# Optimization experiments

Measured on AMD Instinct MI355X. Metric: run time of the kernel, lower is better.

Reference implementation:

```python
import jax, jax.numpy as jnp
import numpy as np

EMBED_DIM = 256
NUM_HEADS = 8
HEAD_DIM = EMBED_DIM // NUM_HEADS
FFN_DIM = 4 * EMBED_DIM
B, N = 2, 2048


def _layernorm(x, w, b, eps=1e-5):
    mu = jnp.mean(x, axis=-1, keepdims=True)
    var = jnp.var(x, axis=-1, keepdims=True)
    return (x - mu) * jax.lax.rsqrt(var + eps) * w + b


def setup_inputs() -> dict:
    key = jax.random.key(0)
    ks = jax.random.split(key, 16)
    s = 0.02
    d = {
        "x": jax.random.normal(ks[0], (B, N, EMBED_DIM), jnp.float32),
        "influence_matrix": jax.random.uniform(ks[1], (B, N, N), jnp.float32),
        "qw": jax.random.normal(ks[2], (EMBED_DIM, EMBED_DIM), jnp.float32) * s,
        "qb": jnp.zeros((EMBED_DIM,), jnp.float32),
        "kw": jax.random.normal(ks[3], (EMBED_DIM, EMBED_DIM), jnp.float32) * s,
        "kb": jnp.zeros((EMBED_DIM,), jnp.float32),
        "vw": jax.random.normal(ks[4], (EMBED_DIM, EMBED_DIM), jnp.float32) * s,
        "vb": jnp.zeros((EMBED_DIM,), jnp.float32),
        "ow": jax.random.normal(ks[5], (EMBED_DIM, EMBED_DIM), jnp.float32) * s,
        "ob": jnp.zeros((EMBED_DIM,), jnp.float32),
        "w1": jax.random.normal(ks[6], (EMBED_DIM, FFN_DIM), jnp.float32) * s,
        "b1": jnp.zeros((FFN_DIM,), jnp.float32),
        "w2": jax.random.normal(ks[7], (FFN_DIM, EMBED_DIM), jnp.float32) * s,
        "b2": jnp.zeros((EMBED_DIM,), jnp.float32),
        "ln1_w": jnp.ones((EMBED_DIM,), jnp.float32),
        "ln1_b": jnp.zeros((EMBED_DIM,), jnp.float32),
        "ln2_w": jnp.ones((EMBED_DIM,), jnp.float32),
        "ln2_b": jnp.zeros((EMBED_DIM,), jnp.float32),
    }
    return d


def reference(x, influence_matrix, qw, qb, kw, kb, vw, vb, ow, ob,
              w1, b1, w2, b2, ln1_w, ln1_b, ln2_w, ln2_b):
    # --- pre-norm attention with multiplicative influence bias ---
    h = _layernorm(x, ln1_w, ln1_b)
    q = (h @ qw + qb).reshape(B, N, NUM_HEADS, HEAD_DIM)
    k = (h @ kw + kb).reshape(B, N, NUM_HEADS, HEAD_DIM)
    v = (h @ vw + vb).reshape(B, N, NUM_HEADS, HEAD_DIM)
    scores = jnp.einsum('bnhd,bmhd->bhnm', q, k) / np.sqrt(HEAD_DIM).astype(np.float32)
    scores = scores * (1.0 + influence_matrix[:, None, :, :])  # multiplicative bias
    attn = jax.nn.softmax(scores, axis=-1)
    out = jnp.einsum('bhnm,bmhd->bnhd', attn, v).reshape(B, N, EMBED_DIM)
    x = x + out @ ow + ob
    # --- GELU FFN (torch GELU is exact erf form) ---
    h2 = _layernorm(x, ln2_w, ln2_b)
    ff = jax.nn.gelu(h2 @ w1 + b1, approximate=False) @ w2 + b2
    return x + ff
```

## Files before the change

kernel.cpp:

```cpp
#include <hip/hip_runtime.h>
#include <hip/hip_bf16.h>
#include <math.h>

#define NSEQ 2048
#define DMODEL 256

typedef __attribute__((ext_vector_type(8))) __bf16 bf16x8;
typedef __attribute__((ext_vector_type(4))) float f32x4;
typedef __attribute__((ext_vector_type(8))) unsigned short ushort8;
typedef __attribute__((ext_vector_type(4))) unsigned int uint4e;

__device__ __forceinline__ unsigned short f2b(float f) {
    return __builtin_bit_cast(unsigned short, (__bf16)f);
}
__device__ __forceinline__ float b2f(unsigned short u) {
    return (float)__builtin_bit_cast(__bf16, u);
}
__device__ __forceinline__ bf16x8 ldfrag16(const void* p) {
    return __builtin_bit_cast(bf16x8, *(const uint4e*)p);
}

__global__ __launch_bounds__(256)
void tr_kernel(const float* __restrict__ in, __bf16* __restrict__ out, int K, int N)
{
    __shared__ float tile[32][33];
    const int tx = threadIdx.x & 31, ty = threadIdx.x >> 5;
    const int n0 = blockIdx.x * 32, k0 = blockIdx.y * 32;
#pragma unroll
    for (int j = 0; j < 4; ++j)
        tile[ty * 4 + j][tx] = in[(size_t)(k0 + ty * 4 + j) * N + n0 + tx];
    __syncthreads();
#pragma unroll
    for (int j = 0; j < 4; ++j)
        out[(size_t)(n0 + ty * 4 + j) * K + k0 + tx] = (__bf16)tile[tx][ty * 4 + j];
}

__global__ __launch_bounds__(256)
void tr4_kernel(const float* __restrict__ w0, const float* __restrict__ w1,
                const float* __restrict__ w2, const float* __restrict__ w3,
                __bf16* __restrict__ o0, __bf16* __restrict__ o1,
                __bf16* __restrict__ o2, __bf16* __restrict__ o3)
{
    __shared__ float tile[32][33];
    const int z = blockIdx.z;
    const float* in = (z == 0) ? w0 : (z == 1) ? w1 : (z == 2) ? w2 : w3;
    __bf16* out     = (z == 0) ? o0 : (z == 1) ? o1 : (z == 2) ? o2 : o3;
    const int tx = threadIdx.x & 31, ty = threadIdx.x >> 5;
    const int n0 = blockIdx.x * 32, k0 = blockIdx.y * 32;
#pragma unroll
    for (int j = 0; j < 4; ++j)
        tile[ty * 4 + j][tx] = in[(size_t)(k0 + ty * 4 + j) * 256 + n0 + tx];
    __syncthreads();
#pragma unroll
    for (int j = 0; j < 4; ++j)
        out[(size_t)(n0 + ty * 4 + j) * 256 + k0 + tx] = (__bf16)tile[tx][ty * 4 + j];
}

__global__ __launch_bounds__(256)
void ln_kernel(const float* __restrict__ x, const float* __restrict__ g,
               const float* __restrict__ b, __bf16* __restrict__ out)
{
    const int row  = blockIdx.x * 4 + (threadIdx.x >> 6);
    const int lane = threadIdx.x & 63;
    const float4 v = *(const float4*)(x + (size_t)row * DMODEL + lane * 4);
    float s  = v.x + v.y + v.z + v.w;
    float s2 = v.x*v.x + v.y*v.y + v.z*v.z + v.w*v.w;
#pragma unroll
    for (int off = 32; off; off >>= 1) {
        s  += __shfl_xor(s, off);
        s2 += __shfl_xor(s2, off);
    }
    const float mu = s * (1.0f / DMODEL);
    const float rs = rsqrtf(s2 * (1.0f / DMODEL) - mu * mu + 1e-5f);
    const float4 gv = *(const float4*)(g + lane * 4);
    const float4 bv = *(const float4*)(b + lane * 4);
    __bf16* o = out + (size_t)row * DMODEL + lane * 4;
    o[0] = (__bf16)((v.x - mu) * rs * gv.x + bv.x);
    o[1] = (__bf16)((v.y - mu) * rs * gv.y + bv.y);
    o[2] = (__bf16)((v.z - mu) * rs * gv.z + bv.z);
    o[3] = (__bf16)((v.w - mu) * rs * gv.w + bv.w);
}

template<int WN>
__device__ __forceinline__ void gemm2_core(
    const __bf16* __restrict__ A, const __bf16* __restrict__ WT,
    const float* __restrict__ bias, const float* __restrict__ resid,
    void* __restrict__ outp, int M, int N, int K, int epi, short* LDSv)
{
    const int t = threadIdx.x, lane = t & 63, w = t >> 6;
    const int g = lane >> 4, c = lane & 15;
    const int row0 = blockIdx.y * 64, col0 = blockIdx.x * WN;

    const __bf16* arow = A  + (size_t)(row0 + w * 16 + c) * K + g * 8;
    const __bf16* brow = WT + (size_t)(col0 + c) * K + g * 8;

    f32x4 acc[WN / 16] = {};
#pragma unroll 8
    for (int k = 0; k < K; k += 32) {
        const bf16x8 a = ldfrag16(arow + k);
#pragma unroll
        for (int dt = 0; dt < WN / 16; ++dt) {
            const bf16x8 bb = ldfrag16(brow + (size_t)dt * 16 * K + k);
            acc[dt] = __builtin_amdgcn_mfma_f32_16x16x32_bf16(a, bb, acc[dt], 0, 0, 0);
        }
    }

    if (epi == 3) {
#pragma unroll
        for (int dt = 0; dt < WN / 16; ++dt)
#pragma unroll
        for (int r = 0; r < 4; ++r)
            LDSv[(dt * 16 + c) * 72 + w * 16 + g * 4 + r] =
                (short)f2b(acc[dt][r] + bias[col0 + dt * 16 + c]);
        __syncthreads();
        const int col = t >> 3, seg = t & 7;
        const uint4e o = *(const uint4e*)&LDSv[col * 72 + seg * 8];
        *(uint4e*)((__bf16*)outp + (size_t)(col0 + col) * M + row0 + seg * 8) = o;
    } else {
#pragma unroll
        for (int dt = 0; dt < WN / 16; ++dt)
#pragma unroll
        for (int r = 0; r < 4; ++r) {
            const int row = row0 + w * 16 + g * 4 + r;
            const int col = col0 + dt * 16 + c;
            float val = acc[dt][r] + bias[col];
            if (epi == 0) {
                ((__bf16*)outp)[(size_t)row * N + col] = (__bf16)val;
            } else if (epi == 1) {
                val = 0.5f * val * (1.0f + erff(val * 0.70710678118654752f));
                ((__bf16*)outp)[(size_t)row * N + col] = (__bf16)val;
            } else {
                ((float*)outp)[(size_t)row * N + col] = resid[(size_t)row * N + col] + val;
            }
        }
    }
}

template<int WN, int EPI>
__global__ __launch_bounds__(256)
void gemm_kernel(const __bf16* __restrict__ A, const __bf16* __restrict__ WT,
                 const float* __restrict__ bias, const float* __restrict__ resid,
                 void* __restrict__ outp, int M, int N, int K)
{
    __shared__ short LDSv[32 * 72];
    gemm2_core<WN>(A, WT, bias, resid, outp, M, N, K, EPI, LDSv);
}

__global__ __launch_bounds__(256)
void qkv_kernel(const __bf16* __restrict__ A,
                const __bf16* __restrict__ qwT, const __bf16* __restrict__ kwT,
                const __bf16* __restrict__ vwT,
                const float* __restrict__ qb, const float* __restrict__ kb,
                const float* __restrict__ vb,
                __bf16* __restrict__ qo, __bf16* __restrict__ ko,
                __bf16* __restrict__ vto)
{
    __shared__ short LDSv[32 * 72];
    const int z = blockIdx.z;
    const __bf16* W    = (z == 0) ? qwT : (z == 1) ? kwT : vwT;
    const float*  bias = (z == 0) ? qb  : (z == 1) ? kb  : vb;
    void* outp         = (z == 0) ? (void*)qo : (z == 1) ? (void*)ko : (void*)vto;
    gemm2_core<32>(A, W, bias, nullptr, outp, 4096, 256, 256, (z == 2) ? 3 : 0, LDSv);
}

__global__ __launch_bounds__(512, 4)
void attn_kernel(const __bf16* __restrict__ Q, const __bf16* __restrict__ K,
                 const __bf16* __restrict__ VT, const float* __restrict__ infl,
                 __bf16* __restrict__ Opart, float* __restrict__ ml)
{
    __shared__ float ilds[2][16][66];
    __shared__ short Pm[8][16][72];

    const int t    = threadIdx.x;
    const int lane = t & 63;
    const int w    = t >> 6;
    const int g    = lane >> 4, c = lane & 15;
    const int b    = blockIdx.z;
    const int sp   = blockIdx.y;
    const int n0   = blockIdx.x * 16;
    const int m_start = sp * 1024;
    const float scale = 0.17677669529663687f;

    const bf16x8 qf = ldfrag16(Q + (size_t)(b * NSEQ + n0 + c) * DMODEL + w * 32 + g * 8);

    const __bf16* Khead = K  + (size_t)(b * NSEQ + c) * DMODEL + w * 32 + g * 8;
    const __bf16* Vhead = VT + (size_t)(w * 32 + c) * (2 * NSEQ) + b * NSEQ + g * 8;

    const int irN = t >> 5, icol = (t & 31) * 2;
    const float* iptr = infl + (size_t)(b * NSEQ + n0 + irN) * NSEQ + icol;

    f32x4 Oacc[2] = {};
    float lsum[4] = {0.f, 0.f, 0.f, 0.f};

    float2 ireg = *(const float2*)(iptr + m_start);
    bf16x8 kf[4];
#pragma unroll
    for (int dt = 0; dt < 4; ++dt)
        kf[dt] = ldfrag16(Khead + (size_t)(m_start + dt * 16) * DMODEL);

    int buf = 0;
    for (int it = 0; it < 16; ++it) {
        const int m0 = m_start + (it << 6);
        const int mn = m_start + (((it + 1) & 15) << 6);

        *(float2*)&ilds[buf][irN][icol] = ireg;
        asm volatile("s_waitcnt lgkmcnt(0)" ::: "memory");
        __builtin_amdgcn_s_barrier();

        ireg = *(const float2*)(iptr + mn);
        bf16x8 kn[4];
#pragma unroll
        for (int dt = 0; dt < 4; ++dt)
            kn[dt] = ldfrag16(Khead + (size_t)(mn + dt * 16) * DMODEL);
        bf16x8 vf[4];
#pragma unroll
        for (int ks = 0; ks < 2; ++ks)
#pragma unroll
            for (int dt = 0; dt < 2; ++dt)
                vf[ks * 2 + dt] =
                    ldfrag16(Vhead + (size_t)(dt * 16) * (2 * NSEQ) + m0 + ks * 32);

        f32x4 s[4];
#pragma unroll
        for (int mt = 0; mt < 4; ++mt) {
            f32x4 z4 = {0.f, 0.f, 0.f, 0.f};
            s[mt] = __builtin_amdgcn_mfma_f32_16x16x32_bf16(qf, kf[mt], z4, 0, 0, 0);
        }

        float p[4][4];
#pragma unroll
        for (int mt = 0; mt < 4; ++mt)
#pragma unroll
            for (int r = 0; r < 4; ++r) {
                const float iw = scale + scale * ilds[buf][g * 4 + r][mt * 16 + c];
                const float pe = __expf(s[mt][r] * iw);
                p[mt][r] = pe;
                lsum[r] += pe;
            }
#pragma unroll
        for (int mt = 0; mt < 4; ++mt)
#pragma unroll
            for (int r = 0; r < 4; ++r)
                Pm[w][g * 4 + r][mt * 16 + c] = (short)f2b(p[mt][r]);
        asm volatile("" ::: "memory");

#pragma unroll
        for (int ks = 0; ks < 2; ++ks) {
            const bf16x8 pf = ldfrag16(&Pm[w][c][ks * 32 + g * 8]);
            Oacc[0] = __builtin_amdgcn_mfma_f32_16x16x32_bf16(pf, vf[ks * 2 + 0], Oacc[0], 0, 0, 0);
            Oacc[1] = __builtin_amdgcn_mfma_f32_16x16x32_bf16(pf, vf[ks * 2 + 1], Oacc[1], 0, 0, 0);
        }

#pragma unroll
        for (int dt = 0; dt < 4; ++dt)
            kf[dt] = kn[dt];
        buf ^= 1;
    }

#pragma unroll
    for (int off = 1; off < 16; off <<= 1)
#pragma unroll
        for (int r = 0; r < 4; ++r)
            lsum[r] += __shfl_xor(lsum[r], off);

    if (c == 0) {
#pragma unroll
        for (int r = 0; r < 4; ++r)
            ml[((size_t)(sp * 4096 + b * NSEQ + n0 + g * 4 + r)) * 8 + w] = lsum[r];
    }

#pragma unroll
    for (int r = 0; r < 4; ++r) {
        const int grow = b * NSEQ + n0 + g * 4 + r;
#pragma unroll
        for (int dt = 0; dt < 2; ++dt)
            Opart[(size_t)(sp * 4096 + grow) * 256 + w * 32 + dt * 16 + c] =
                (__bf16)Oacc[dt][r];
    }
}

__global__ __launch_bounds__(256)
void combine_kernel(const __bf16* __restrict__ Opart, const float* __restrict__ ml,
                    __bf16* __restrict__ ao)
{
    const int tid = blockIdx.x * 256 + threadIdx.x;
    const int row = tid >> 5;
    const int d0  = (tid & 31) * 8;
    const int h   = d0 >> 5;
    const float l0 = ml[(size_t)row * 8 + h];
    const float l1 = ml[(size_t)(4096 + row) * 8 + h];
    const float inv = 1.0f / (l0 + l1);
    const ushort8 xa = *(const ushort8*)(Opart + (size_t)row * 256 + d0);
    const ushort8 xb = *(const ushort8*)(Opart + (size_t)(4096 + row) * 256 + d0);
    __bf16 o[8];
#pragma unroll
    for (int e = 0; e < 8; ++e)
        o[e] = (__bf16)((b2f(xa[e]) + b2f(xb[e])) * inv);
    *(uint4e*)(ao + (size_t)row * 256 + d0) = *(uint4e*)o;
}

extern "C" void kernel_launch(void* const* d_in, const int* in_sizes, int n_in,
                              void* d_out, int out_size, void* d_ws, size_t ws_size,
                              hipStream_t stream)
{
    (void)in_sizes; (void)n_in; (void)out_size; (void)ws_size;
    const float* x    = (const float*)d_in[0];
    const float* infl = (const float*)d_in[1];
    const float* qw   = (const float*)d_in[2];
    const float* qb   = (const float*)d_in[3];
    const float* kw   = (const float*)d_in[4];
    const float* kb   = (const float*)d_in[5];
    const float* vw   = (const float*)d_in[6];
    const float* vb   = (const float*)d_in[7];
    const float* ow   = (const float*)d_in[8];
    const float* ob_  = (const float*)d_in[9];
    const float* w1   = (const float*)d_in[10];
    const float* b1   = (const float*)d_in[11];
    const float* w2   = (const float*)d_in[12];
    const float* b2   = (const float*)d_in[13];
    const float* ln1w = (const float*)d_in[14];
    const float* ln1b = (const float*)d_in[15];
    const float* ln2w = (const float*)d_in[16];
    const float* ln2b = (const float*)d_in[17];
    float* out = (float*)d_out;

    char* ws = (char*)d_ws;
    __bf16* qwT   = (__bf16*)(ws);
    __bf16* kwT   = (__bf16*)(ws + (128u << 10));
    __bf16* vwT   = (__bf16*)(ws + (256u << 10));
    __bf16* owT   = (__bf16*)(ws + (384u << 10));
    __bf16* w1T   = (__bf16*)(ws + (512u << 10));
    __bf16* w2T   = (__bf16*)(ws + (1024u << 10));
    __bf16* h     = (__bf16*)(ws +  2 * 1048576ull);
    __bf16* q     = (__bf16*)(ws +  4 * 1048576ull);
    __bf16* kx    = (__bf16*)(ws +  6 * 1048576ull);
    __bf16* vt    = (__bf16*)(ws +  8 * 1048576ull);
    __bf16* Opart = (__bf16*)(ws + 10 * 1048576ull);
    float*  mlbuf = (float*) (ws + 14 * 1048576ull);
    __bf16* ao    = (__bf16*)(ws + 15 * 1048576ull);
    float*  x2    = (float*) (ws + 17 * 1048576ull);
    __bf16* h2    = (__bf16*)(ws + 21 * 1048576ull);
    __bf16* ff    = (__bf16*)(ws + 23 * 1048576ull);

    tr4_kernel<<<dim3(8, 8, 4),  256, 0, stream>>>(qw, kw, vw, ow, qwT, kwT, vwT, owT);
    tr_kernel <<<dim3(32, 8),    256, 0, stream>>>(w1, w1T, 256, 1024);
    tr_kernel <<<dim3(8, 32),    256, 0, stream>>>(w2, w2T, 1024, 256);

    ln_kernel<<<1024, 256, 0, stream>>>(x, ln1w, ln1b, h);
    qkv_kernel<<<dim3(8, 64, 3), 256, 0, stream>>>(h, qwT, kwT, vwT, qb, kb, vb, q, kx, vt);
    attn_kernel<<<dim3(128, 2, 2), 512, 0, stream>>>(q, kx, vt, infl, Opart, mlbuf);
    combine_kernel<<<512, 256, 0, stream>>>(Opart, mlbuf, ao);
    gemm_kernel<32, 2><<<dim3(8, 64),  256, 0, stream>>>(ao, owT, ob_, x,      x2,  4096,  256,  256);
    ln_kernel<<<1024, 256, 0, stream>>>(x2, ln2w, ln2b, h2);
    gemm_kernel<64, 1><<<dim3(16, 64), 256, 0, stream>>>(h2, w1T, b1, nullptr, ff,  4096, 1024,  256);
    gemm_kernel<32, 2><<<dim3(8, 64),  256, 0, stream>>>(ff, w2T, b2, x2,     out, 4096,  256, 1024);
}
```

Baseline: 255.5 us.

## Fuse layernorms into GEMMs, stage weights in LDS, split attention four ways

Merges the three weight-transpose launches into one prep kernel. Fuses both layernorms into the QKV and FFN1 GEMMs, which normalise rows straight into LDS. Every projection GEMM moves to 64x64 tiles with weight panels staged in padded shared memory. The attention key range is split into four chunks of 512 instead of two of 1024 for more blocks, and the combine kernel sums four partials. This cuts launches and intermediate HBM traffic and raises attention parallelism, at the cost of more LDS per block, redundant layernorm work across column tiles, and more partial-result traffic.

```diff
diff --git a/kernel.cpp b/kernel.cpp
--- a/kernel.cpp
+++ b/kernel.cpp
@@ -4,6 +4,7 @@
 
 #define NSEQ 2048
 #define DMODEL 256
+#define STRD 296
 
 typedef __attribute__((ext_vector_type(8))) __bf16 bf16x8;
 typedef __attribute__((ext_vector_type(4))) float f32x4;
@@ -19,13 +20,42 @@
 __device__ __forceinline__ bf16x8 ldfrag16(const void* p) {
     return __builtin_bit_cast(bf16x8, *(const uint4e*)p);
 }
-
-__global__ __launch_bounds__(256)
-void tr_kernel(const float* __restrict__ in, __bf16* __restrict__ out, int K, int N)
+__device__ __forceinline__ uint4e pack8(float a0,float a1,float a2,float a3,
+                                        float b0,float b1,float b2,float b3) {
+    uint4e u;
+    u.x = (unsigned)f2b(a0) | ((unsigned)f2b(a1) << 16);
+    u.y = (unsigned)f2b(a2) | ((unsigned)f2b(a3) << 16);
+    u.z = (unsigned)f2b(b0) | ((unsigned)f2b(b1) << 16);
+    u.w = (unsigned)f2b(b2) | ((unsigned)f2b(b3) << 16);
+    return u;
+}
+
+__global__ __launch_bounds__(256)
+void prep_kernel(const float* __restrict__ qw, const float* __restrict__ kw,
+                 const float* __restrict__ vw, const float* __restrict__ ow,
+                 const float* __restrict__ w1, const float* __restrict__ w2,
+                 __bf16* __restrict__ qwT, __bf16* __restrict__ kwT,
+                 __bf16* __restrict__ vwT, __bf16* __restrict__ owT,
+                 __bf16* __restrict__ w1T, __bf16* __restrict__ w2T)
 {
     __shared__ float tile[32][33];
+    const int b = blockIdx.x;
+    const float* in; __bf16* out; int K, N, k0, n0;
+    if (b < 256) {
+        const int wsel = b >> 6, tl = b & 63;
+        in  = (wsel == 0) ? qw  : (wsel == 1) ? kw  : (wsel == 2) ? vw  : ow;
+        out = (wsel == 0) ? qwT : (wsel == 1) ? kwT : (wsel == 2) ? vwT : owT;
+        K = 256; N = 256; k0 = (tl >> 3) * 32; n0 = (tl & 7) * 32;
+    } else if (b < 512) {
+        const int tl = b - 256;
+        in = w1; out = w1T; K = 256; N = 1024;
+        k0 = (tl >> 5) * 32; n0 = (tl & 31) * 32;
+    } else {
+        const int tl = b - 512;
+        in = w2; out = w2T; K = 1024; N = 256;
+        k0 = (tl >> 3) * 32; n0 = (tl & 7) * 32;
+    }
     const int tx = threadIdx.x & 31, ty = threadIdx.x >> 5;
-    const int n0 = blockIdx.x * 32, k0 = blockIdx.y * 32;
 #pragma unroll
     for (int j = 0; j < 4; ++j)
         tile[ty * 4 + j][tx] = in[(size_t)(k0 + ty * 4 + j) * N + n0 + tx];
@@ -35,119 +65,58 @@
         out[(size_t)(n0 + ty * 4 + j) * K + k0 + tx] = (__bf16)tile[tx][ty * 4 + j];
 }
 
-__global__ __launch_bounds__(256)
-void tr4_kernel(const float* __restrict__ w0, const float* __restrict__ w1,
-                const float* __restrict__ w2, const float* __restrict__ w3,
-                __bf16* __restrict__ o0, __bf16* __restrict__ o1,
-                __bf16* __restrict__ o2, __bf16* __restrict__ o3)
-{
-    __shared__ float tile[32][33];
-    const int z = blockIdx.z;
-    const float* in = (z == 0) ? w0 : (z == 1) ? w1 : (z == 2) ? w2 : w3;
-    __bf16* out     = (z == 0) ? o0 : (z == 1) ? o1 : (z == 2) ? o2 : o3;
-    const int tx = threadIdx.x & 31, ty = threadIdx.x >> 5;
-    const int n0 = blockIdx.x * 32, k0 = blockIdx.y * 32;
-#pragma unroll
-    for (int j = 0; j < 4; ++j)
-        tile[ty * 4 + j][tx] = in[(size_t)(k0 + ty * 4 + j) * 256 + n0 + tx];
-    __syncthreads();
-#pragma unroll
-    for (int j = 0; j < 4; ++j)
-        out[(size_t)(n0 + ty * 4 + j) * 256 + k0 + tx] = (__bf16)tile[tx][ty * 4 + j];
-}
-
-__global__ __launch_bounds__(256)
-void ln_kernel(const float* __restrict__ x, const float* __restrict__ g,
-               const float* __restrict__ b, __bf16* __restrict__ out)
-{
-    const int row  = blockIdx.x * 4 + (threadIdx.x >> 6);
-    const int lane = threadIdx.x & 63;
-    const float4 v = *(const float4*)(x + (size_t)row * DMODEL + lane * 4);
-    float s  = v.x + v.y + v.z + v.w;
-    float s2 = v.x*v.x + v.y*v.y + v.z*v.z + v.w*v.w;
-#pragma unroll
-    for (int off = 32; off; off >>= 1) {
-        s  += __shfl_xor(s, off);
-        s2 += __shfl_xor(s2, off);
-    }
-    const float mu = s * (1.0f / DMODEL);
-    const float rs = rsqrtf(s2 * (1.0f / DMODEL) - mu * mu + 1e-5f);
-    const float4 gv = *(const float4*)(g + lane * 4);
-    const float4 bv = *(const float4*)(b + lane * 4);
-    __bf16* o = out + (size_t)row * DMODEL + lane * 4;
-    o[0] = (__bf16)((v.x - mu) * rs * gv.x + bv.x);
-    o[1] = (__bf16)((v.y - mu) * rs * gv.y + bv.y);
-    o[2] = (__bf16)((v.z - mu) * rs * gv.z + bv.z);
-    o[3] = (__bf16)((v.w - mu) * rs * gv.w + bv.w);
-}
-
-template<int WN>
-__device__ __forceinline__ void gemm2_core(
-    const __bf16* __restrict__ A, const __bf16* __restrict__ WT,
-    const float* __restrict__ bias, const float* __restrict__ resid,
-    void* __restrict__ outp, int M, int N, int K, int epi, short* LDSv)
-{
-    const int t = threadIdx.x, lane = t & 63, w = t >> 6;
-    const int g = lane >> 4, c = lane & 15;
-    const int row0 = blockIdx.y * 64, col0 = blockIdx.x * WN;
-
-    const __bf16* arow = A  + (size_t)(row0 + w * 16 + c) * K + g * 8;
-    const __bf16* brow = WT + (size_t)(col0 + c) * K + g * 8;
-
-    f32x4 acc[WN / 16] = {};
-#pragma unroll 8
-    for (int k = 0; k < K; k += 32) {
-        const bf16x8 a = ldfrag16(arow + k);
-#pragma unroll
-        for (int dt = 0; dt < WN / 16; ++dt) {
-            const bf16x8 bb = ldfrag16(brow + (size_t)dt * 16 * K + k);
-            acc[dt] = __builtin_amdgcn_mfma_f32_16x16x32_bf16(a, bb, acc[dt], 0, 0, 0);
-        }
-    }
-
-    if (epi == 3) {
-#pragma unroll
-        for (int dt = 0; dt < WN / 16; ++dt)
-#pragma unroll
-        for (int r = 0; r < 4; ++r)
-            LDSv[(dt * 16 + c) * 72 + w * 16 + g * 4 + r] =
-                (short)f2b(acc[dt][r] + bias[col0 + dt * 16 + c]);
-        __syncthreads();
-        const int col = t >> 3, seg = t & 7;
-        const uint4e o = *(const uint4e*)&LDSv[col * 72 + seg * 8];
-        *(uint4e*)((__bf16*)outp + (size_t)(col0 + col) * M + row0 + seg * 8) = o;
-    } else {
-#pragma unroll
-        for (int dt = 0; dt < WN / 16; ++dt)
-#pragma unroll
-        for (int r = 0; r < 4; ++r) {
-            const int row = row0 + w * 16 + g * 4 + r;
-            const int col = col0 + dt * 16 + c;
-            float val = acc[dt][r] + bias[col];
-            if (epi == 0) {
-                ((__bf16*)outp)[(size_t)row * N + col] = (__bf16)val;
-            } else if (epi == 1) {
-                val = 0.5f * val * (1.0f + erff(val * 0.70710678118654752f));
-                ((__bf16*)outp)[(size_t)row * N + col] = (__bf16)val;
-            } else {
-                ((float*)outp)[(size_t)row * N + col] = resid[(size_t)row * N + col] + val;
-            }
-        }
-    }
-}
-
-template<int WN, int EPI>
-__global__ __launch_bounds__(256)
-void gemm_kernel(const __bf16* __restrict__ A, const __bf16* __restrict__ WT,
-                 const float* __restrict__ bias, const float* __restrict__ resid,
-                 void* __restrict__ outp, int M, int N, int K)
-{
-    __shared__ short LDSv[32 * 72];
-    gemm2_core<WN>(A, WT, bias, resid, outp, M, N, K, EPI, LDSv);
-}
-
-__global__ __launch_bounds__(256)
-void qkv_kernel(const __bf16* __restrict__ A,
+__device__ __forceinline__ void stage_panel(const __bf16* __restrict__ src, int ldk,
+                                            int col0, int kbase, short* dst)
+{
+    const int t = threadIdx.x;
+#pragma unroll
+    for (int i = 0; i < 8; ++i) {
+        const int flat = i * 256 + t;
+        const int row = flat >> 5, seg = flat & 31;
+        *(uint4e*)(dst + row * STRD + seg * 8) =
+            *(const uint4e*)(src + (size_t)(col0 + row) * ldk + kbase + seg * 8);
+    }
+}
+
+__device__ __forceinline__ void ln_to_lds(const float* __restrict__ xrow0,
+                                          const float* __restrict__ lw,
+                                          const float* __restrict__ lb, short* As)
+{
+    const int t = threadIdx.x;
+    const int r = t >> 2, q = t & 3;
+    const float* xp = xrow0 + (size_t)r * 256 + q * 64;
+    float4 v[16];
+    float s = 0.f, s2 = 0.f;
+#pragma unroll
+    for (int j = 0; j < 16; ++j) {
+        v[j] = *(const float4*)(xp + j * 4);
+        s  += v[j].x + v[j].y + v[j].z + v[j].w;
+        s2 += v[j].x*v[j].x + v[j].y*v[j].y + v[j].z*v[j].z + v[j].w*v[j].w;
+    }
+    s  += __shfl_xor(s, 1);  s  += __shfl_xor(s, 2);
+    s2 += __shfl_xor(s2, 1); s2 += __shfl_xor(s2, 2);
+    const float mu = s * (1.0f / 256.0f);
+    const float rs = rsqrtf(s2 * (1.0f / 256.0f) - mu * mu + 1e-5f);
+    const float* gw = lw + q * 64;
+    const float* gb = lb + q * 64;
+#pragma unroll
+    for (int j = 0; j < 8; ++j) {
+        const float4 w0 = *(const float4*)(gw + j * 8);
+        const float4 w1 = *(const float4*)(gw + j * 8 + 4);
+        const float4 b0 = *(const float4*)(gb + j * 8);
+        const float4 b1 = *(const float4*)(gb + j * 8 + 4);
+        const float4 a = v[j * 2], bq = v[j * 2 + 1];
+        *(uint4e*)(As + r * STRD + q * 64 + j * 8) = pack8(
+            (a.x - mu) * rs * w0.x + b0.x, (a.y - mu) * rs * w0.y + b0.y,
+            (a.z - mu) * rs * w0.z + b0.z, (a.w - mu) * rs * w0.w + b0.w,
+            (bq.x - mu) * rs * w1.x + b1.x, (bq.y - mu) * rs * w1.y + b1.y,
+            (bq.z - mu) * rs * w1.z + b1.z, (bq.w - mu) * rs * w1.w + b1.w);
+    }
+}
+
+__global__ __launch_bounds__(256)
+void qkv_kernel(const float* __restrict__ x,
+                const float* __restrict__ lw, const float* __restrict__ lb,
                 const __bf16* __restrict__ qwT, const __bf16* __restrict__ kwT,
                 const __bf16* __restrict__ vwT,
                 const float* __restrict__ qb, const float* __restrict__ kb,
@@ -155,12 +124,169 @@
                 __bf16* __restrict__ qo, __bf16* __restrict__ ko,
                 __bf16* __restrict__ vto)
 {
-    __shared__ short LDSv[32 * 72];
+    __shared__ short As[64 * STRD];
+    __shared__ short Ws[64 * STRD];
     const int z = blockIdx.z;
-    const __bf16* W    = (z == 0) ? qwT : (z == 1) ? kwT : vwT;
-    const float*  bias = (z == 0) ? qb  : (z == 1) ? kb  : vb;
-    void* outp         = (z == 0) ? (void*)qo : (z == 1) ? (void*)ko : (void*)vto;
-    gemm2_core<32>(A, W, bias, nullptr, outp, 4096, 256, 256, (z == 2) ? 3 : 0, LDSv);
+    const __bf16* WT  = (z == 0) ? qwT : (z == 1) ? kwT : vwT;
+    const float* bias = (z == 0) ? qb  : (z == 1) ? kb  : vb;
+    const int row0 = blockIdx.y * 64, col0 = blockIdx.x * 64;
+
+    ln_to_lds(x + (size_t)row0 * 256, lw, lb, As);
+    stage_panel(WT, 256, col0, 0, Ws);
+    __syncthreads();
+
+    const int t = threadIdx.x, lane = t & 63, w = t >> 6;
+    const int g = lane >> 4, c = lane & 15;
+    const short* ap = As + (w * 16 + c) * STRD + g * 8;
+    const short* bp = Ws + c * STRD + g * 8;
+    f32x4 acc[4] = {};
+#pragma unroll
+    for (int kc = 0; kc < 256; kc += 32) {
+        const bf16x8 a = ldfrag16(ap + kc);
+#pragma unroll
+        for (int dt = 0; dt < 4; ++dt) {
+            const bf16x8 bb = ldfrag16(bp + dt * 16 * STRD + kc);
+            acc[dt] = __builtin_amdgcn_mfma_f32_16x16x32_bf16(a, bb, acc[dt], 0, 0, 0);
+        }
+    }
+
+    if (z == 2) {
+        __syncthreads();
+        short* LT = Ws;
+#pragma unroll
+        for (int dt = 0; dt < 4; ++dt)
+#pragma unroll
+        for (int r = 0; r < 4; ++r)
+            LT[(dt * 16 + c) * 72 + w * 16 + g * 4 + r] =
+                (short)f2b(acc[dt][r] + bias[col0 + dt * 16 + c]);
+        __syncthreads();
+        const int col = t >> 2;
+#pragma unroll
+        for (int i = 0; i < 2; ++i) {
+            const int seg = (t & 3) * 2 + i;
+            *(uint4e*)(vto + (size_t)(col0 + col) * 4096 + row0 + seg * 8) =
+                *(const uint4e*)&LT[col * 72 + seg * 8];
+        }
+    } else {
+        __bf16* o = (z == 0) ? qo : ko;
+#pragma unroll
+        for (int dt = 0; dt < 4; ++dt)
+#pragma unroll
+        for (int r = 0; r < 4; ++r) {
+            const int row = row0 + w * 16 + g * 4 + r;
+            const int col = col0 + dt * 16 + c;
+            o[(size_t)row * 256 + col] = (__bf16)(acc[dt][r] + bias[col]);
+        }
+    }
+}
+
+__global__ __launch_bounds__(256)
+void oproj_kernel(const __bf16* __restrict__ ao, const __bf16* __restrict__ owT,
+                  const float* __restrict__ ob, const float* __restrict__ x,
+                  float* __restrict__ x2)
+{
+    __shared__ short Ws[64 * STRD];
+    const int row0 = blockIdx.y * 64, col0 = blockIdx.x * 64;
+    stage_panel(owT, 256, col0, 0, Ws);
+    __syncthreads();
+    const int t = threadIdx.x, lane = t & 63, w = t >> 6;
+    const int g = lane >> 4, c = lane & 15;
+    const __bf16* arow = ao + (size_t)(row0 + w * 16 + c) * 256 + g * 8;
+    const short* bp = Ws + c * STRD + g * 8;
+    f32x4 acc[4] = {};
+#pragma unroll
+    for (int kc = 0; kc < 256; kc += 32) {
+        const bf16x8 a = ldfrag16(arow + kc);
+#pragma unroll
+        for (int dt = 0; dt < 4; ++dt) {
+            const bf16x8 bb = ldfrag16(bp + dt * 16 * STRD + kc);
+            acc[dt] = __builtin_amdgcn_mfma_f32_16x16x32_bf16(a, bb, acc[dt], 0, 0, 0);
+        }
+    }
+#pragma unroll
+    for (int dt = 0; dt < 4; ++dt)
+#pragma unroll
+    for (int r = 0; r < 4; ++r) {
+        const int row = row0 + w * 16 + g * 4 + r;
+        const int col = col0 + dt * 16 + c;
+        x2[(size_t)row * 256 + col] =
+            x[(size_t)row * 256 + col] + acc[dt][r] + ob[col];
+    }
+}
+
+__global__ __launch_bounds__(256)
+void ffn1_kernel(const float* __restrict__ x2,
+                 const float* __restrict__ lw, const float* __restrict__ lb,
+                 const __bf16* __restrict__ w1T, const float* __restrict__ b1,
+                 __bf16* __restrict__ ff)
+{
+    __shared__ short As[64 * STRD];
+    __shared__ short Ws[64 * STRD];
+    const int row0 = blockIdx.y * 64, col0 = blockIdx.x * 64;
+    ln_to_lds(x2 + (size_t)row0 * 256, lw, lb, As);
+    stage_panel(w1T, 256, col0, 0, Ws);
+    __syncthreads();
+    const int t = threadIdx.x, lane = t & 63, w = t >> 6;
+    const int g = lane >> 4, c = lane & 15;
+    const short* ap = As + (w * 16 + c) * STRD + g * 8;
+    const short* bp = Ws + c * STRD + g * 8;
+    f32x4 acc[4] = {};
+#pragma unroll
+    for (int kc = 0; kc < 256; kc += 32) {
+        const bf16x8 a = ldfrag16(ap + kc);
+#pragma unroll
+        for (int dt = 0; dt < 4; ++dt) {
+            const bf16x8 bb = ldfrag16(bp + dt * 16 * STRD + kc);
+            acc[dt] = __builtin_amdgcn_mfma_f32_16x16x32_bf16(a, bb, acc[dt], 0, 0, 0);
+        }
+    }
+#pragma unroll
+    for (int dt = 0; dt < 4; ++dt)
+#pragma unroll
+    for (int r = 0; r < 4; ++r) {
+        const int row = row0 + w * 16 + g * 4 + r;
+        const int col = col0 + dt * 16 + c;
+        float val = acc[dt][r] + b1[col];
+        val = 0.5f * val * (1.0f + erff(val * 0.70710678118654752f));
+        ff[(size_t)row * 1024 + col] = (__bf16)val;
+    }
+}
+
+__global__ __launch_bounds__(256)
+void ffn2_kernel(const __bf16* __restrict__ ff, const __bf16* __restrict__ w2T,
+                 const float* __restrict__ b2, const float* __restrict__ x2,
+                 float* __restrict__ out)
+{
+    __shared__ short Ws[64 * STRD];
+    const int row0 = blockIdx.y * 64, col0 = blockIdx.x * 64;
+    const int t = threadIdx.x, lane = t & 63, w = t >> 6;
+    const int g = lane >> 4, c = lane & 15;
+    const __bf16* arow = ff + (size_t)(row0 + w * 16 + c) * 1024 + g * 8;
+    const short* bp = Ws + c * STRD + g * 8;
+    f32x4 acc[4] = {};
+    for (int ck = 0; ck < 4; ++ck) {
+        if (ck) __syncthreads();
+        stage_panel(w2T, 1024, col0, ck * 256, Ws);
+        __syncthreads();
+#pragma unroll
+        for (int kc = 0; kc < 256; kc += 32) {
+            const bf16x8 a = ldfrag16(arow + ck * 256 + kc);
+#pragma unroll
+            for (int dt = 0; dt < 4; ++dt) {
+                const bf16x8 bb = ldfrag16(bp + dt * 16 * STRD + kc);
+                acc[dt] = __builtin_amdgcn_mfma_f32_16x16x32_bf16(a, bb, acc[dt], 0, 0, 0);
+            }
+        }
+    }
+#pragma unroll
+    for (int dt = 0; dt < 4; ++dt)
+#pragma unroll
+    for (int r = 0; r < 4; ++r) {
+        const int row = row0 + w * 16 + g * 4 + r;
+        const int col = col0 + dt * 16 + c;
+        out[(size_t)row * 256 + col] =
+            x2[(size_t)row * 256 + col] + acc[dt][r] + b2[col];
+    }
 }
 
 __global__ __launch_bounds__(512, 4)
@@ -169,7 +295,7 @@
                  __bf16* __restrict__ Opart, float* __restrict__ ml)
 {
     __shared__ float ilds[2][16][66];
-    __shared__ short Pm[8][16][72];
+    __shared__ short Pm[8][16][104];
 
     const int t    = threadIdx.x;
     const int lane = t & 63;
@@ -178,7 +304,7 @@
     const int b    = blockIdx.z;
     const int sp   = blockIdx.y;
     const int n0   = blockIdx.x * 16;
-    const int m_start = sp * 1024;
+    const int m_start = sp * 512;
     const float scale = 0.17677669529663687f;
 
     const bf16x8 qf = ldfrag16(Q + (size_t)(b * NSEQ + n0 + c) * DMODEL + w * 32 + g * 8);
@@ -199,9 +325,9 @@
         kf[dt] = ldfrag16(Khead + (size_t)(m_start + dt * 16) * DMODEL);
 
     int buf = 0;
-    for (int it = 0; it < 16; ++it) {
+    for (int it = 0; it < 8; ++it) {
         const int m0 = m_start + (it << 6);
-        const int mn = m_start + (((it + 1) & 15) << 6);
+        const int mn = m_start + (((it + 1) & 7) << 6);
 
         *(float2*)&ilds[buf][irN][icol] = ireg;
         asm volatile("s_waitcnt lgkmcnt(0)" ::: "memory");
@@ -287,15 +413,21 @@
     const int row = tid >> 5;
     const int d0  = (tid & 31) * 8;
     const int h   = d0 >> 5;
-    const float l0 = ml[(size_t)row * 8 + h];
-    const float l1 = ml[(size_t)(4096 + row) * 8 + h];
-    const float inv = 1.0f / (l0 + l1);
-    const ushort8 xa = *(const ushort8*)(Opart + (size_t)row * 256 + d0);
-    const ushort8 xb = *(const ushort8*)(Opart + (size_t)(4096 + row) * 256 + d0);
+    float l = 0.f;
+#pragma unroll
+    for (int sp = 0; sp < 4; ++sp)
+        l += ml[((size_t)(sp * 4096 + row)) * 8 + h];
+    const float inv = 1.0f / l;
+    float acc[8] = {};
+#pragma unroll
+    for (int sp = 0; sp < 4; ++sp) {
+        const ushort8 xp = *(const ushort8*)(Opart + ((size_t)(sp * 4096 + row)) * 256 + d0);
+#pragma unroll
+        for (int e = 0; e < 8; ++e) acc[e] += b2f(xp[e]);
+    }
     __bf16 o[8];
 #pragma unroll
-    for (int e = 0; e < 8; ++e)
-        o[e] = (__bf16)((b2f(xa[e]) + b2f(xb[e])) * inv);
+    for (int e = 0; e < 8; ++e) o[e] = (__bf16)(acc[e] * inv);
     *(uint4e*)(ao + (size_t)row * 256 + d0) = *(uint4e*)o;
 }
 
@@ -331,27 +463,22 @@
     __bf16* owT   = (__bf16*)(ws + (384u << 10));
     __bf16* w1T   = (__bf16*)(ws + (512u << 10));
     __bf16* w2T   = (__bf16*)(ws + (1024u << 10));
-    __bf16* h     = (__bf16*)(ws +  2 * 1048576ull);
-    __bf16* q     = (__bf16*)(ws +  4 * 1048576ull);
-    __bf16* kx    = (__bf16*)(ws +  6 * 1048576ull);
-    __bf16* vt    = (__bf16*)(ws +  8 * 1048576ull);
-    __bf16* Opart = (__bf16*)(ws + 10 * 1048576ull);
-    float*  mlbuf = (float*) (ws + 14 * 1048576ull);
-    __bf16* ao    = (__bf16*)(ws + 15 * 1048576ull);
-    float*  x2    = (float*) (ws + 17 * 1048576ull);
-    __bf16* h2    = (__bf16*)(ws + 21 * 1048576ull);
+    __bf16* q     = (__bf16*)(ws +  2 * 1048576ull);
+    __bf16* kx    = (__bf16*)(ws +  4 * 1048576ull);
+    __bf16* vt    = (__bf16*)(ws +  6 * 1048576ull);
+    __bf16* Opart = (__bf16*)(ws +  8 * 1048576ull);
+    float*  mlbuf = (float*) (ws + 16 * 1048576ull);
+    __bf16* ao    = (__bf16*)(ws + 17 * 1048576ull);
+    float*  x2    = (float*) (ws + 19 * 1048576ull);
     __bf16* ff    = (__bf16*)(ws + 23 * 1048576ull);
 
-    tr4_kernel<<<dim3(8, 8, 4),  256, 0, stream>>>(qw, kw, vw, ow, qwT, kwT, vwT, owT);
-    tr_kernel <<<dim3(32, 8),    256, 0, stream>>>(w1, w1T, 256, 1024);
-    tr_kernel <<<dim3(8, 32),    256, 0, stream>>>(w2, w2T, 1024, 256);
-
-    ln_kernel<<<1024, 256, 0, stream>>>(x, ln1w, ln1b, h);
-    qkv_kernel<<<dim3(8, 64, 3), 256, 0, stream>>>(h, qwT, kwT, vwT, qb, kb, vb, q, kx, vt);
-    attn_kernel<<<dim3(128, 2, 2), 512, 0, stream>>>(q, kx, vt, infl, Opart, mlbuf);
+    prep_kernel<<<768, 256, 0, stream>>>(qw, kw, vw, ow, w1, w2,
+                                         qwT, kwT, vwT, owT, w1T, w2T);
+    qkv_kernel<<<dim3(4, 64, 3), 256, 0, stream>>>(x, ln1w, ln1b, qwT, kwT, vwT,
+                                                   qb, kb, vb, q, kx, vt);
+    attn_kernel<<<dim3(128, 4, 2), 512, 0, stream>>>(q, kx, vt, infl, Opart, mlbuf);
     combine_kernel<<<512, 256, 0, stream>>>(Opart, mlbuf, ao);
-    gemm_kernel<32, 2><<<dim3(8, 64),  256, 0, stream>>>(ao, owT, ob_, x,      x2,  4096,  256,  256);
-    ln_kernel<<<1024, 256, 0, stream>>>(x2, ln2w, ln2b, h2);
-    gemm_kernel<64, 1><<<dim3(16, 64), 256, 0, stream>>>(h2, w1T, b1, nullptr, ff,  4096, 1024,  256);
-    gemm_kernel<32, 2><<<dim3(8, 64),  256, 0, stream>>>(ff, w2T, b2, x2,     out, 4096,  256, 1024);
-}
+    oproj_kernel<<<dim3(4, 64), 256, 0, stream>>>(ao, owT, ob_, x, x2);
+    ffn1_kernel<<<dim3(16, 64), 256, 0, stream>>>(x2, ln2w, ln2b, w1T, b1, ff);
+    ffn2_kernel<<<dim3(4, 64), 256, 0, stream>>>(ff, w2T, b2, x2, out);
+}
```

Result: faster. 238.0 us (-6.8%).
